# Performance work log

Hardware: AMD Instinct MI355X
Metric: run time of the kernel (lower is better)

Reference implementation:

```python
import jax, jax.numpy as jnp
import numpy as np

S = 16   # source_num (sorted axis length)
H = 4    # heads
N = 128  # batch
D = 512  # feature dim


def _source_index(s):
    # row c (for bcode c+1): entry j = j+1 if bit j of (c+1) is set else 0
    codes = np.arange(1, 2 ** s, dtype=np.int64)
    bits = (codes[:, None] >> np.arange(s)) & 1          # (2^s-1, s), LSB-first
    return jnp.asarray(bits * (np.arange(s) + 1), dtype=jnp.int32)


def setup_inputs() -> dict:
    key = jax.random.key(0)
    k1, k2, k3 = jax.random.split(key, 3)
    x = jax.random.normal(k1, (N, S, D), dtype=jnp.float32)
    # FM: row 0 is the fixed zero row ('source absent'), rows 1..S learned
    FM = jnp.concatenate([jnp.zeros((1, H), jnp.float32),
                          jax.random.normal(k2, (S, H), dtype=jnp.float32)], axis=0)
    Agg = jax.random.normal(k3, (1, S, H), dtype=jnp.float32)
    return {"x": x, "FM": FM, "Agg": Agg, "source_index": _source_index(S)}


def reference(x, FM, Agg, source_index):
    n, s, d = x.shape
    # descending sort along source axis
    idx = jnp.argsort(-x, axis=1)                        # (N,S,D) ints in [0,S)
    x_sort = jnp.take_along_axis(x, idx, axis=1)
    # gap encoding: consecutive differences, last gap = last value - 0
    gaps = jnp.concatenate([x_sort[:, :-1] - x_sort[:, 1:], x_sort[:, -1:]], axis=1)
    # combinatorial code of the top-k set at each sort position
    codes = jnp.cumsum(jnp.power(2, idx).astype(jnp.int32), axis=1) - 1  # (N,S,D) in [0, 2^S-2]
    # precompute per-code reduction: table[c] = sum_j FM[source_index[c, j]] * Agg[0, j]
    # identical math to (FM[source_index[codes]] * Agg).sum(1) but avoids the huge gather
    table = jnp.einsum('cjh,jh->ch', FM[source_index], Agg[0])  # (2^S-1, H)
    fm = table[codes]                                    # (N,S,D,H)
    out = jnp.einsum('nsd,nsdh->ndh', gaps, fm)          # weighted reduce over sort axis
    return jnp.transpose(out, (0, 2, 1))                 # concat=True -> (N,H,D)
```

## Files before the change

### kernel.cpp

```cpp
#include <hip/hip_runtime.h>


#define CIE_S 16
#define CIE_H 4
#define CIE_N 128
#define CIE_D 512
#define CIE_D4 (CIE_D / 4)

__global__ __launch_bounds__(64)
void CIE_18236431138961_kernel(const float* __restrict__ x,
                               const float* __restrict__ FM,
                               const float* __restrict__ Agg,
                               float* __restrict__ out) {
    const int t  = blockIdx.x * 64 + threadIdx.x;
    const int n  = t / CIE_D4;
    const int d4 = t % CIE_D4;

    float W[CIE_S][CIE_H];
#pragma unroll
    for (int j = 0; j < CIE_S; ++j) {
#pragma unroll
        for (int h = 0; h < CIE_H; ++h) {
            W[j][h] = FM[(j + 1) * CIE_H + h] * Agg[j * CIE_H + h];
        }
    }

    const float4* __restrict__ x4   = (const float4*)x;
    float4* __restrict__       out4 = (float4*)out;

    float4 acc[CIE_H];
#pragma unroll
    for (int h = 0; h < CIE_H; ++h) acc[h] = make_float4(0.f, 0.f, 0.f, 0.f);

#pragma unroll
    for (int j = 0; j < CIE_S; ++j) {
        const float4 v = x4[(n * CIE_S + j) * CIE_D4 + d4];
#pragma unroll
        for (int h = 0; h < CIE_H; ++h) {
            acc[h].x += W[j][h] * v.x;
            acc[h].y += W[j][h] * v.y;
            acc[h].z += W[j][h] * v.z;
            acc[h].w += W[j][h] * v.w;
        }
    }

#pragma unroll
    for (int h = 0; h < CIE_H; ++h) {
        out4[(n * CIE_H + h) * CIE_D4 + d4] = acc[h];
    }
}

extern "C" void kernel_launch(void* const* d_in, const int* in_sizes, int n_in,
                              void* d_out, int out_size, void* d_ws, size_t ws_size,
                              hipStream_t stream) {
    const float* x   = (const float*)d_in[0];
    const float* FM  = (const float*)d_in[1];
    const float* Agg = (const float*)d_in[2];
    float* out = (float*)d_out;

    const int total  = CIE_N * CIE_D4;
    const int block  = 64;
    const int grid   = total / block;

    CIE_18236431138961_kernel<<<grid, block, 0, stream>>>(x, FM, Agg, out);
}
```

Baseline: 61.09 us.

## Split source-axis reduction across four waves with LDS combine

Each block now runs four waves. Each wave handles a quarter of the 16 source rows for the same 64 output elements. Waves 1-3 write partial sums to shared memory, and wave 0 adds them up and writes the output after a barrier. The aim is more waves in flight and more concurrent loads, to hide memory latency in an otherwise small grid. In exchange it adds LDS traffic, a block-wide barrier, and three waves that sit idle during the final combine.

After: 61.75 us. About the same (+1.1%).

```diff
diff --git a/kernel.cpp b/kernel.cpp
--- a/kernel.cpp
+++ b/kernel.cpp
@@ -6,47 +6,72 @@
 #define CIE_N 128
 #define CIE_D 512
 #define CIE_D4 (CIE_D / 4)
+#define CIE_WAVES 4
+#define CIE_JPW (CIE_S / CIE_WAVES)
 
-__global__ __launch_bounds__(64)
+__global__ __launch_bounds__(256)
 void CIE_18236431138961_kernel(const float* __restrict__ x,
                                const float* __restrict__ FM,
                                const float* __restrict__ Agg,
                                float* __restrict__ out) {
-    const int t  = blockIdx.x * 64 + threadIdx.x;
-    const int n  = t / CIE_D4;
-    const int d4 = t % CIE_D4;
+    __shared__ float4 lds[CIE_H][CIE_WAVES - 1][64];
 
-    float W[CIE_S][CIE_H];
+    const int tid  = threadIdx.x;
+    const int w    = tid >> 6;
+    const int lane = tid & 63;
+    const int e    = blockIdx.x * 64 + lane;
+    const int n    = e / CIE_D4;
+    const int d4   = e % CIE_D4;
+
+    const int j0 = w * CIE_JPW;
+    float W[CIE_JPW][CIE_H];
 #pragma unroll
-    for (int j = 0; j < CIE_S; ++j) {
+    for (int jj = 0; jj < CIE_JPW; ++jj) {
 #pragma unroll
         for (int h = 0; h < CIE_H; ++h) {
-            W[j][h] = FM[(j + 1) * CIE_H + h] * Agg[j * CIE_H + h];
+            W[jj][h] = FM[(j0 + jj + 1) * CIE_H + h] * Agg[(j0 + jj) * CIE_H + h];
         }
     }
 
-    const float4* __restrict__ x4   = (const float4*)x;
-    float4* __restrict__       out4 = (float4*)out;
+    const float4* __restrict__ x4 = (const float4*)x;
 
     float4 acc[CIE_H];
 #pragma unroll
     for (int h = 0; h < CIE_H; ++h) acc[h] = make_float4(0.f, 0.f, 0.f, 0.f);
 
 #pragma unroll
-    for (int j = 0; j < CIE_S; ++j) {
-        const float4 v = x4[(n * CIE_S + j) * CIE_D4 + d4];
+    for (int jj = 0; jj < CIE_JPW; ++jj) {
+        const float4 v = x4[(n * CIE_S + j0 + jj) * CIE_D4 + d4];
 #pragma unroll
         for (int h = 0; h < CIE_H; ++h) {
-            acc[h].x += W[j][h] * v.x;
-            acc[h].y += W[j][h] * v.y;
-            acc[h].z += W[j][h] * v.z;
-            acc[h].w += W[j][h] * v.w;
+            acc[h].x += W[jj][h] * v.x;
+            acc[h].y += W[jj][h] * v.y;
+            acc[h].z += W[jj][h] * v.z;
+            acc[h].w += W[jj][h] * v.w;
         }
     }
 
+    if (w != 0) {
 #pragma unroll
-    for (int h = 0; h < CIE_H; ++h) {
-        out4[(n * CIE_H + h) * CIE_D4 + d4] = acc[h];
+        for (int h = 0; h < CIE_H; ++h) lds[h][w - 1][lane] = acc[h];
+    }
+    __syncthreads();
+
+    if (w == 0) {
+#pragma unroll
+        for (int h = 0; h < CIE_H; ++h) {
+#pragma unroll
+            for (int ww = 0; ww < CIE_WAVES - 1; ++ww) {
+                const float4 p = lds[h][ww][lane];
+                acc[h].x += p.x; acc[h].y += p.y;
+                acc[h].z += p.z; acc[h].w += p.w;
+            }
+        }
+        float4* __restrict__ out4 = (float4*)out;
+#pragma unroll
+        for (int h = 0; h < CIE_H; ++h) {
+            out4[(n * CIE_H + h) * CIE_D4 + d4] = acc[h];
+        }
     }
 }
 
@@ -58,9 +83,8 @@
     const float* Agg = (const float*)d_in[2];
     float* out = (float*)d_out;
 
-    const int total  = CIE_N * CIE_D4;
-    const int block  = 64;
-    const int grid   = total / block;
+    const int total = CIE_N * CIE_D4;
+    const int grid  = total / 64;
 
-    CIE_18236431138961_kernel<<<grid, block, 0, stream>>>(x, FM, Agg, out);
+    CIE_18236431138961_kernel<<<grid, 256, 0, stream>>>(x, FM, Agg, out);
 }
```
